# Kernel optimization log

Hardware: AMD Instinct MI355X
Metric: run time of the kernel (lower is better)

Reference implementation:

```python
import jax, jax.numpy as jnp
import numpy as np

TEMP = 1.0
EULER_GAMMA = 0.5772156649015329
BIG = 1.0e9


def setup_inputs() -> dict:
    key = jax.random.key(0)
    k = jax.random.split(key, 8)
    B, N, D, H = 32, 1024, 1024, 512  # batch, seq, d_model, hidden_size//2
    queries = jax.random.normal(k[0], (B, N, D), jnp.float32)
    queries_mask = jnp.ones((B, N), dtype=bool)
    W1 = jax.random.normal(k[1], (D, H), jnp.float32) * 0.02
    b1 = jnp.zeros((H,), jnp.float32)
    W2 = jax.random.normal(k[2], (H, 1), jnp.float32) * 0.02
    b2 = jnp.zeros((1,), jnp.float32)
    uniform_noise = jax.random.uniform(k[3], (B, N, 1), jnp.float32, 0.0, 1e-5)
    gumbel_noise = jax.random.gumbel(k[4], (B, N, 1), jnp.float32)
    return {"queries": queries, "queries_mask": queries_mask, "W1": W1, "b1": b1,
            "W2": W2, "b2": b2, "uniform_noise": uniform_noise,
            "gumbel_noise": gumbel_noise, "action_refinement": 1}


def reference(queries, queries_mask, W1, b1, W2, b2, uniform_noise, gumbel_noise, action_refinement):
    B, N, D = queries.shape
    # block0: Dense(H, relu) -> Dense(1); then softplus clamp + log + tiny uniform noise
    h = jax.nn.relu(jnp.einsum('bnd,dh->bnh', queries, W1) + b1)
    acts = jnp.einsum('bnh,ho->bno', h, W2) + b2                      # [B,N,1]
    acts = jnp.log(jnp.maximum(jax.nn.softplus(acts), 1e-5)) + uniform_noise
    acts = jnp.repeat(acts, action_refinement, axis=0)                # [BR,N,1]
    vmask = jnp.repeat(queries_mask[:, None, :].astype(jnp.float32), action_refinement, axis=0)  # [BR,1,N]
    n_valid = jnp.sum(vmask, axis=-1)                                 # [BR,1]
    mask_n1 = jnp.transpose(vmask, (0, 2, 1))                         # [BR,N,1]
    sqz_mask = mask_n1[..., 0]                                        # [BR,N]
    masked_acts = jnp.where(mask_n1 > 0, acts, -1e6)                  # [BR,N,1]
    perturb = masked_acts + gumbel_noise                              # [BR,N,1]
    # deterministic NeuralSort
    s = (jnp.exp(perturb) * mask_n1)[..., 0]                          # [BR,N]
    A = jnp.abs(s[:, :, None] - s[:, None, :])                        # [BR,N,N]
    Bmat = jnp.sum(A, axis=-1, keepdims=True)                         # A @ (1 1^T): row sums broadcast
    scaling = (N + 1 - 2 * (jnp.arange(N) + 1)).astype(jnp.float32)   # [N]
    C = s[:, :, None] * scaling[None, None, :]                        # [BR,N,N]
    P_hat = jnp.transpose(C - Bmat, (0, 2, 1)) - (1.0 - vmask) * BIG  # [BR,N,N]
    # greedy argmax permutation extraction (find_permu), vectorized over batch
    BR = P_hat.shape[0]
    def step(flag, row):                                              # row: [BR,N]
        tmp = row - flag * BIG
        idx = jnp.argmax(tmp, axis=-1)
        flag = jnp.maximum(flag, jax.nn.one_hot(idx, N, dtype=flag.dtype))
        return flag, idx
    _, idxs = jax.lax.scan(step, jnp.zeros((BR, N), jnp.float32), jnp.transpose(P_hat, (1, 0, 2)))
    chosen = jnp.transpose(idxs).astype(jnp.int32)                    # [BR,N]
    chosen = jnp.concatenate([jnp.zeros((BR, 1), jnp.int32), chosen[:, :-1]], axis=-1)
    id_permu = jnp.arange(N, dtype=jnp.int32)[None, :]
    permu = jnp.where(sqz_mask > 0, chosen, id_permu)                 # [BR,N]
    sample_permu = jax.nn.one_hot(permu, N, axis=-1, dtype=jnp.float32)
    # Plackett-Luce log-likelihood of sampled permutation
    exp_actis = jnp.exp(jnp.take_along_axis(masked_acts[..., 0], permu, axis=-1))
    rev_cumsum = jnp.cumsum(exp_actis[:, ::-1], axis=-1)[:, ::-1]
    eps = 1e-20
    log_nom = (jnp.log(exp_actis + eps) - jnp.log(rev_cumsum + eps)) * sqz_mask
    log_nom = jnp.sum(log_nom, axis=-1, keepdims=True)                # [BR,1]
    log_norm = jnp.zeros_like(log_nom)
    # KL term
    sqz_acts = acts[..., 0]
    kl1 = n_valid * (np.log(TEMP) - 1.0 + EULER_GAMMA * (1.0 / TEMP - 1.0))
    s1 = (1.0 / TEMP) * jnp.sum(sqz_acts * sqz_mask, axis=-1).reshape(-1, 1)
    s2 = jnp.sum(jnp.exp(-1.0 / TEMP * jnp.maximum(sqz_acts * sqz_mask, -20.0 * TEMP)), axis=-1).reshape(-1, 1) - (jnp.float32(N) - n_valid)
    kl = kl1 + s1 + s2 * jnp.exp(jax.lax.lgamma(jnp.float32(1.0 + 1.0 / TEMP)))
    return sample_permu, masked_acts[..., 0], kl, log_nom, log_norm
```

## Files before the change

kernel.cpp:

```cpp
#include <hip/hip_runtime.h>
#include <math.h>

#define BB 32
#define NN 1024
#define DD 1024
#define HH 512

#define OUT0_OFF 0
#define OUT1_OFF (BB * NN * NN)
#define OUT2_OFF (OUT1_OFF + BB * NN)
#define OUT3_OFF (OUT2_OFF + BB)
#define OUT4_OFF (OUT3_OFF + BB)

#define WS_ACTS 0
#define WS_W1T  131072
#define WS_RANK 1179648

typedef __attribute__((ext_vector_type(8))) short short8;
typedef __attribute__((ext_vector_type(4))) float floatx4;

__device__ inline unsigned int f2bf(float x) {
    unsigned int u = __builtin_bit_cast(unsigned int, x);
    return (u + 0x7FFFu + ((u >> 16) & 1u)) >> 16;
}

__global__ __launch_bounds__(1024) void w1t_kernel(const float* __restrict__ W1,
                                                   unsigned short* __restrict__ W1T)
{
    __shared__ float T[32][33];
    const int tx = threadIdx.x, ty = threadIdx.y;
    const int d0 = blockIdx.x * 32, h0 = blockIdx.y * 32;
    T[ty][tx] = W1[(d0 + ty) * HH + h0 + tx];
    __syncthreads();
    W1T[(size_t)(h0 + ty) * DD + d0 + tx] = (unsigned short)f2bf(T[tx][ty]);
}

#define ASTRIDE 40
__global__ __launch_bounds__(256, 2) void gemm_acts_kernel(
    const float* __restrict__ q, const unsigned short* __restrict__ W1T,
    const float* __restrict__ b1, const float* __restrict__ W2,
    const float* __restrict__ b2, const float* __restrict__ unoise,
    float* __restrict__ acts_ws, float* __restrict__ out1)
{
    __shared__ short As[64 * ASTRIDE];
    __shared__ short Bs[512 * ASTRIDE];
    __shared__ float red[64][4];

    const int tid = threadIdx.x;
    const int w = tid >> 6;
    const int lane = tid & 63;
    const int c = lane & 15;
    const int qd = lane >> 4;
    const int m0 = blockIdx.x * 64;

    float b1v[8], w2v[8];
    #pragma unroll
    for (int tn = 0; tn < 8; ++tn) {
        int col = w * 128 + tn * 16 + c;
        b1v[tn] = b1[col];
        w2v[tn] = W2[col];
    }

    floatx4 acc[8][4];
    #pragma unroll
    for (int tn = 0; tn < 8; ++tn)
        #pragma unroll
        for (int tm = 0; tm < 4; ++tm)
            acc[tn][tm] = (floatx4){0.f, 0.f, 0.f, 0.f};

    const int am = tid >> 2;
    const int akf = (tid & 3) * 8;
    const float* aptr = q + (size_t)(m0 + am) * DD + akf;

    const uint4* w1t4 = (const uint4*)W1T;

    for (int kk = 0; kk < 32; ++kk) {
        __syncthreads();
        {
            const float4* ap = (const float4*)(aptr + kk * 32);
            float4 v0 = ap[0], v1 = ap[1];
            uint4 pk;
            pk.x = f2bf(v0.x) | (f2bf(v0.y) << 16);
            pk.y = f2bf(v0.z) | (f2bf(v0.w) << 16);
            pk.z = f2bf(v1.x) | (f2bf(v1.y) << 16);
            pk.w = f2bf(v1.z) | (f2bf(v1.w) << 16);
            *(uint4*)(&As[am * ASTRIDE + akf]) = pk;
        }
        #pragma unroll
        for (int i = 0; i < 8; ++i) {
            int f = i * 256 + tid;
            int n = f >> 2, kp = f & 3;
            uint4 v = w1t4[(size_t)n * 128 + kk * 4 + kp];
            *(uint4*)(&Bs[n * ASTRIDE + kp * 8]) = v;
        }
        __syncthreads();
        short8 af[4];
        #pragma unroll
        for (int tm = 0; tm < 4; ++tm)
            af[tm] = *(const short8*)(&As[(tm * 16 + c) * ASTRIDE + qd * 8]);
        #pragma unroll
        for (int tn = 0; tn < 8; ++tn) {
            short8 bf = *(const short8*)(&Bs[(w * 128 + tn * 16 + c) * ASTRIDE + qd * 8]);
            #pragma unroll
            for (int tm = 0; tm < 4; ++tm)
                acc[tn][tm] = __builtin_amdgcn_mfma_f32_16x16x32_bf16(
                    af[tm], bf, acc[tn][tm], 0, 0, 0);
        }
    }

    #pragma unroll
    for (int tm = 0; tm < 4; ++tm) {
        #pragma unroll
        for (int r = 0; r < 4; ++r) {
            float p = 0.f;
            #pragma unroll
            for (int tn = 0; tn < 8; ++tn) {
                float v = acc[tn][tm][r] + b1v[tn];
                p = fmaf(fmaxf(v, 0.f), w2v[tn], p);
            }
            p += __shfl_xor(p, 1);
            p += __shfl_xor(p, 2);
            p += __shfl_xor(p, 4);
            p += __shfl_xor(p, 8);
            if (c == 0) red[tm * 16 + qd * 4 + r][w] = p;
        }
    }
    __syncthreads();
    if (tid < 64) {
        float raw = red[tid][0] + red[tid][1] + red[tid][2] + red[tid][3] + b2[0];
        float sp = fmaxf(raw, 0.f) + log1pf(expf(-fabsf(raw)));
        int row = m0 + tid;
        float av = logf(fmaxf(sp, 1e-5f)) + unoise[row];
        acts_ws[row] = av;
        out1[row]    = av;
    }
}

__global__ __launch_bounds__(256) void zero_kernel(float4* __restrict__ p, int n4)
{
    int idx = blockIdx.x * blockDim.x + threadIdx.x;
    int stride = gridDim.x * blockDim.x;
    float4 z = make_float4(0.f, 0.f, 0.f, 0.f);
    for (int i = idx; i < n4; i += stride) p[i] = z;
}

__global__ __launch_bounds__(256) void rank_kernel(
    const float* __restrict__ acts_ws, const float* __restrict__ gumbel,
    int* __restrict__ rank)
{
    __shared__ float P[NN];
    const int b = blockIdx.x >> 2;
    const int chunk = blockIdx.x & 3;
    const int tid = threadIdx.x;
    #pragma unroll
    for (int r = 0; r < 4; ++r) {
        int j = r * 256 + tid;
        P[j] = acts_ws[b * NN + j] + gumbel[b * NN + j];
    }
    __syncthreads();
    const int i = chunk * 256 + tid;
    const float pert = P[i];
    int cnt = 0;
    const float4* P4 = (const float4*)P;
    for (int j4 = 0; j4 < NN / 4; ++j4) {
        float4 pv = P4[j4];
        int j = j4 * 4;
        cnt += (pv.x > pert) || (pv.x == pert && j + 0 < i);
        cnt += (pv.y > pert) || (pv.y == pert && j + 1 < i);
        cnt += (pv.z > pert) || (pv.z == pert && j + 2 < i);
        cnt += (pv.w > pert) || (pv.w == pert && j + 3 < i);
    }
    rank[b * NN + i] = cnt;
}

__global__ __launch_bounds__(1024) void permu_stats_kernel(
    const float* __restrict__ acts_ws, const int* __restrict__ rank,
    float* __restrict__ out0, float* __restrict__ out2,
    float* __restrict__ out3, float* __restrict__ out4)
{
    __shared__ float A[NN];
    __shared__ int   IDX[NN];
    __shared__ float S[NN];
    __shared__ float R[NN];

    const int b = blockIdx.x;
    const int i = threadIdx.x;

    float a = acts_ws[b * NN + i];
    A[i] = a;
    IDX[rank[b * NN + i]] = i;
    __syncthreads();

    int perm = (i == 0) ? 0 : IDX[i - 1];
    out0[((size_t)b * NN + i) * NN + perm] = 1.0f;

    float e = expf(A[perm]);
    S[i] = e;
    __syncthreads();
    #pragma unroll
    for (int off = 1; off < NN; off <<= 1) {
        float v = (i + off < NN) ? S[i + off] : 0.f;
        __syncthreads();
        S[i] += v;
        __syncthreads();
    }
    float term = logf(e + 1e-20f) - logf(S[i] + 1e-20f);

    float lognom = 0.f, s1 = 0.f;
    R[i] = term;
    __syncthreads();
    #pragma unroll
    for (int off = 512; off > 0; off >>= 1) {
        if (i < off) R[i] += R[i + off];
        __syncthreads();
    }
    if (i == 0) lognom = R[0];
    R[i] = a;
    __syncthreads();
    #pragma unroll
    for (int off = 512; off > 0; off >>= 1) {
        if (i < off) R[i] += R[i + off];
        __syncthreads();
    }
    if (i == 0) s1 = R[0];
    R[i] = expf(-fmaxf(a, -20.f));
    __syncthreads();
    #pragma unroll
    for (int off = 512; off > 0; off >>= 1) {
        if (i < off) R[i] += R[i + off];
        __syncthreads();
    }
    if (i == 0) {
        float s2 = R[0];
        out2[b] = -(float)NN + s1 + s2;
        out3[b] = lognom;
        out4[b] = 0.f;
    }
}

extern "C" void kernel_launch(void* const* d_in, const int* in_sizes, int n_in,
                              void* d_out, int out_size, void* d_ws, size_t ws_size,
                              hipStream_t stream)
{
    const float* q      = (const float*)d_in[0];
    const float* W1     = (const float*)d_in[2];
    const float* b1     = (const float*)d_in[3];
    const float* W2     = (const float*)d_in[4];
    const float* b2     = (const float*)d_in[5];
    const float* unoise = (const float*)d_in[6];
    const float* gumbel = (const float*)d_in[7];

    float* out  = (float*)d_out;
    char*  ws   = (char*)d_ws;
    float*          acts = (float*)(ws + WS_ACTS);
    unsigned short* W1T  = (unsigned short*)(ws + WS_W1T);
    int*            rank = (int*)(ws + WS_RANK);

    w1t_kernel<<<dim3(32, 16), dim3(32, 32), 0, stream>>>(W1, W1T);
    gemm_acts_kernel<<<(BB * NN) / 64, 256, 0, stream>>>(q, W1T, b1, W2, b2,
                                                         unoise, acts,
                                                         out + OUT1_OFF);
    zero_kernel<<<8192, 256, 0, stream>>>((float4*)(out + OUT0_OFF),
                                          (BB * NN * NN) / 4);
    rank_kernel<<<BB * 4, 256, 0, stream>>>(acts, gumbel, rank);
    permu_stats_kernel<<<BB, 1024, 0, stream>>>(acts, rank,
                                                out + OUT0_OFF, out + OUT2_OFF,
                                                out + OUT3_OFF, out + OUT4_OFF);
}
```

Baseline: 325.9 us.

## Load GEMM B fragments directly to registers, fuse one-hot write, use warp-shuffle scans

The GEMM no longer stages W1T through LDS. Each lane loads its bf16 B fragments straight from global memory into registers and prefetches the next k-step, and the A tile is double-buffered so one barrier per iteration is dropped. The separate zero-fill plus scatter of the 128 MB one-hot output becomes a single kernel that writes each row exactly once. The permutation stats kernel now uses wave shuffles for its suffix scan and reductions instead of many LDS barrier passes. The trade-offs are more global load traffic per wave, since B is no longer shared across the block, and higher register pressure.

```diff
diff --git a/kernel.cpp b/kernel.cpp
--- a/kernel.cpp
+++ b/kernel.cpp
@@ -42,15 +42,12 @@
     const float* __restrict__ b2, const float* __restrict__ unoise,
     float* __restrict__ acts_ws, float* __restrict__ out1)
 {
-    __shared__ short As[64 * ASTRIDE];
-    __shared__ short Bs[512 * ASTRIDE];
+    __shared__ short As[2][64 * ASTRIDE];
     __shared__ float red[64][4];
 
     const int tid = threadIdx.x;
-    const int w = tid >> 6;
-    const int lane = tid & 63;
-    const int c = lane & 15;
-    const int qd = lane >> 4;
+    const int w = tid >> 6, lane = tid & 63;
+    const int c = lane & 15, qd = lane >> 4;
     const int m0 = blockIdx.x * 64;
 
     float b1v[8], w2v[8];
@@ -68,14 +65,17 @@
         for (int tm = 0; tm < 4; ++tm)
             acc[tn][tm] = (floatx4){0.f, 0.f, 0.f, 0.f};
 
-    const int am = tid >> 2;
-    const int akf = (tid & 3) * 8;
+    const int am = tid >> 2, akf = (tid & 3) * 8;
     const float* aptr = q + (size_t)(m0 + am) * DD + akf;
 
-    const uint4* w1t4 = (const uint4*)W1T;
+    const unsigned short* bptr = W1T + (size_t)(w * 128 + c) * DD + qd * 8;
+
+    uint4 bfrag[8];
+    #pragma unroll
+    for (int tn = 0; tn < 8; ++tn)
+        bfrag[tn] = *(const uint4*)(bptr + (size_t)tn * 16 * DD);
 
     for (int kk = 0; kk < 32; ++kk) {
-        __syncthreads();
         {
             const float4* ap = (const float4*)(aptr + kk * 32);
             float4 v0 = ap[0], v1 = ap[1];
@@ -84,27 +84,30 @@
             pk.y = f2bf(v0.z) | (f2bf(v0.w) << 16);
             pk.z = f2bf(v1.x) | (f2bf(v1.y) << 16);
             pk.w = f2bf(v1.z) | (f2bf(v1.w) << 16);
-            *(uint4*)(&As[am * ASTRIDE + akf]) = pk;
-        }
-        #pragma unroll
-        for (int i = 0; i < 8; ++i) {
-            int f = i * 256 + tid;
-            int n = f >> 2, kp = f & 3;
-            uint4 v = w1t4[(size_t)n * 128 + kk * 4 + kp];
-            *(uint4*)(&Bs[n * ASTRIDE + kp * 8]) = v;
+            *(uint4*)(&As[kk & 1][am * ASTRIDE + akf]) = pk;
+        }
+        uint4 bnext[8];
+        if (kk < 31) {
+            #pragma unroll
+            for (int tn = 0; tn < 8; ++tn)
+                bnext[tn] = *(const uint4*)(bptr + (size_t)tn * 16 * DD + (kk + 1) * 32);
         }
         __syncthreads();
         short8 af[4];
         #pragma unroll
         for (int tm = 0; tm < 4; ++tm)
-            af[tm] = *(const short8*)(&As[(tm * 16 + c) * ASTRIDE + qd * 8]);
+            af[tm] = *(const short8*)(&As[kk & 1][(tm * 16 + c) * ASTRIDE + qd * 8]);
         #pragma unroll
         for (int tn = 0; tn < 8; ++tn) {
-            short8 bf = *(const short8*)(&Bs[(w * 128 + tn * 16 + c) * ASTRIDE + qd * 8]);
+            short8 bf = __builtin_bit_cast(short8, bfrag[tn]);
             #pragma unroll
             for (int tm = 0; tm < 4; ++tm)
                 acc[tn][tm] = __builtin_amdgcn_mfma_f32_16x16x32_bf16(
                     af[tm], bf, acc[tn][tm], 0, 0, 0);
+        }
+        if (kk < 31) {
+            #pragma unroll
+            for (int tn = 0; tn < 8; ++tn) bfrag[tn] = bnext[tn];
         }
     }
 
@@ -134,14 +137,6 @@
         acts_ws[row] = av;
         out1[row]    = av;
     }
-}
-
-__global__ __launch_bounds__(256) void zero_kernel(float4* __restrict__ p, int n4)
-{
-    int idx = blockIdx.x * blockDim.x + threadIdx.x;
-    int stride = gridDim.x * blockDim.x;
-    float4 z = make_float4(0.f, 0.f, 0.f, 0.f);
-    for (int i = idx; i < n4; i += stride) p[i] = z;
 }
 
 __global__ __launch_bounds__(256) void rank_kernel(
@@ -174,67 +169,75 @@
 }
 
 __global__ __launch_bounds__(1024) void permu_stats_kernel(
-    const float* __restrict__ acts_ws, const int* __restrict__ rank,
-    float* __restrict__ out0, float* __restrict__ out2,
-    float* __restrict__ out3, float* __restrict__ out4)
+    const float* __restrict__ acts_ws, int* __restrict__ rank_perm,
+    float* __restrict__ out2, float* __restrict__ out3, float* __restrict__ out4)
 {
     __shared__ float A[NN];
     __shared__ int   IDX[NN];
-    __shared__ float S[NN];
-    __shared__ float R[NN];
-
-    const int b = blockIdx.x;
-    const int i = threadIdx.x;
+    __shared__ float WT[16];
+    __shared__ float RS[48];
+
+    const int b = blockIdx.x, i = threadIdx.x;
+    const int lane = i & 63, w = i >> 6;
 
     float a = acts_ws[b * NN + i];
     A[i] = a;
-    IDX[rank[b * NN + i]] = i;
+    IDX[rank_perm[b * NN + i]] = i;
     __syncthreads();
 
     int perm = (i == 0) ? 0 : IDX[i - 1];
-    out0[((size_t)b * NN + i) * NN + perm] = 1.0f;
+    rank_perm[b * NN + i] = perm;
 
     float e = expf(A[perm]);
-    S[i] = e;
-    __syncthreads();
-    #pragma unroll
-    for (int off = 1; off < NN; off <<= 1) {
-        float v = (i + off < NN) ? S[i + off] : 0.f;
-        __syncthreads();
-        S[i] += v;
-        __syncthreads();
-    }
-    float term = logf(e + 1e-20f) - logf(S[i] + 1e-20f);
-
-    float lognom = 0.f, s1 = 0.f;
-    R[i] = term;
-    __syncthreads();
-    #pragma unroll
-    for (int off = 512; off > 0; off >>= 1) {
-        if (i < off) R[i] += R[i + off];
-        __syncthreads();
-    }
-    if (i == 0) lognom = R[0];
-    R[i] = a;
-    __syncthreads();
-    #pragma unroll
-    for (int off = 512; off > 0; off >>= 1) {
-        if (i < off) R[i] += R[i + off];
-        __syncthreads();
-    }
-    if (i == 0) s1 = R[0];
-    R[i] = expf(-fmaxf(a, -20.f));
-    __syncthreads();
-    #pragma unroll
-    for (int off = 512; off > 0; off >>= 1) {
-        if (i < off) R[i] += R[i + off];
-        __syncthreads();
-    }
+
+    float s = e;
+    #pragma unroll
+    for (int off = 1; off < 64; off <<= 1) {
+        float v = __shfl_down(s, off);
+        if (lane + off < 64) s += v;
+    }
+    if (lane == 0) WT[w] = s;
+    __syncthreads();
+    float suff = 0.f;
+    for (int ww = w + 1; ww < 16; ++ww) suff += WT[ww];
+    float S = s + suff;
+    float term = logf(e + 1e-20f) - logf(S + 1e-20f);
+
+    float r0 = term, r1 = a, r2 = expf(-fmaxf(a, -20.f));
+    #pragma unroll
+    for (int off = 32; off > 0; off >>= 1) {
+        r0 += __shfl_down(r0, off);
+        r1 += __shfl_down(r1, off);
+        r2 += __shfl_down(r2, off);
+    }
+    if (lane == 0) { RS[w] = r0; RS[16 + w] = r1; RS[32 + w] = r2; }
+    __syncthreads();
     if (i == 0) {
-        float s2 = R[0];
-        out2[b] = -(float)NN + s1 + s2;
-        out3[b] = lognom;
+        float t0 = 0.f, t1 = 0.f, t2 = 0.f;
+        for (int ww = 0; ww < 16; ++ww) {
+            t0 += RS[ww]; t1 += RS[16 + ww]; t2 += RS[32 + ww];
+        }
+        out2[b] = -(float)NN + t1 + t2;
+        out3[b] = t0;
         out4[b] = 0.f;
+    }
+}
+
+__global__ __launch_bounds__(256) void onehot_kernel(
+    const int* __restrict__ perm, float4* __restrict__ out0)
+{
+    const int t = threadIdx.x;
+    const size_t row0 = (size_t)blockIdx.x * 16;
+    #pragma unroll
+    for (int r = 0; r < 16; ++r) {
+        int p = perm[row0 + r];
+        float on = ((p >> 2) == t) ? 1.0f : 0.0f;
+        float4 v;
+        v.x = ((p & 3) == 0) ? on : 0.0f;
+        v.y = ((p & 3) == 1) ? on : 0.0f;
+        v.z = ((p & 3) == 2) ? on : 0.0f;
+        v.w = ((p & 3) == 3) ? on : 0.0f;
+        out0[(row0 + r) * 256 + t] = v;
     }
 }
 
@@ -250,20 +253,18 @@
     const float* unoise = (const float*)d_in[6];
     const float* gumbel = (const float*)d_in[7];
 
-    float* out  = (float*)d_out;
-    char*  ws   = (char*)d_ws;
+    float* out = (float*)d_out;
+    char*  ws  = (char*)d_ws;
     float*          acts = (float*)(ws + WS_ACTS);
     unsigned short* W1T  = (unsigned short*)(ws + WS_W1T);
-    int*            rank = (int*)(ws + WS_RANK);
+    int*            rkpm = (int*)(ws + WS_RANK);
 
     w1t_kernel<<<dim3(32, 16), dim3(32, 32), 0, stream>>>(W1, W1T);
     gemm_acts_kernel<<<(BB * NN) / 64, 256, 0, stream>>>(q, W1T, b1, W2, b2,
                                                          unoise, acts,
                                                          out + OUT1_OFF);
-    zero_kernel<<<8192, 256, 0, stream>>>((float4*)(out + OUT0_OFF),
-                                          (BB * NN * NN) / 4);
-    rank_kernel<<<BB * 4, 256, 0, stream>>>(acts, gumbel, rank);
-    permu_stats_kernel<<<BB, 1024, 0, stream>>>(acts, rank,
-                                                out + OUT0_OFF, out + OUT2_OFF,
+    rank_kernel<<<BB * 4, 256, 0, stream>>>(acts, gumbel, rkpm);
+    permu_stats_kernel<<<BB, 1024, 0, stream>>>(acts, rkpm, out + OUT2_OFF,
                                                 out + OUT3_OFF, out + OUT4_OFF);
-}
+    onehot_kernel<<<2048, 256, 0, stream>>>(rkpm, (float4*)(out + OUT0_OFF));
+}
```

Measured after the change: 340.3 us. 1.04x slower.
